# Kernel tuning notes

Measured on AMD Instinct MI355X. Metric: run time of the kernel, lower is better.

The kernel has to match this reference:

```python
import jax, jax.numpy as jnp
import numpy as np

HIDDEN = 2048
FFN = 1024
NUM_EXPERTS = 64
TOP_K = 8
TOTAL_EXPERTS = NUM_EXPERTS + TOP_K  # trash-can experts appended


def setup_inputs() -> dict:
    key = jax.random.key(0)
    ks = jax.random.split(key, 5)
    hidden_states = jax.random.normal(ks[0], (4, 2048, HIDDEN), dtype=jnp.float32)
    # gate: [total_experts, hidden]
    gate_w = jax.random.normal(ks[1], (TOTAL_EXPERTS, HIDDEN), dtype=jnp.float32) * 0.02
    # OlmoeMLP (SwiGLU): gate_proj, up_proj: [E, hidden, ffn]; down_proj: [E, ffn, hidden]
    w_gate = jax.random.normal(ks[2], (NUM_EXPERTS, HIDDEN, FFN), dtype=jnp.float32) * 0.02
    w_up = jax.random.normal(ks[3], (NUM_EXPERTS, HIDDEN, FFN), dtype=jnp.float32) * 0.02
    w_down = jax.random.normal(ks[4], (NUM_EXPERTS, FFN, HIDDEN), dtype=jnp.float32) * 0.02
    return {"hidden_states": hidden_states, "gate_w": gate_w,
            "w_gate": w_gate, "w_up": w_up, "w_down": w_down}


def _moe_forward(hidden_states, gate_w, w_gate, w_up, w_down):
    b, s, h = hidden_states.shape
    x = hidden_states.reshape(-1, h)  # [T, H]
    router_logits = x @ gate_w.T  # [T, total_experts]
    routing_weights = jax.nn.softmax(router_logits.astype(jnp.float32), axis=-1)
    topk_w, topk_idx = jax.lax.top_k(routing_weights, TOP_K)  # [T, K]
    # norm_topk_prob = False -> no renorm
    topk_w = topk_w.astype(hidden_states.dtype)

    # Dense-equivalent combine honoring sparsity via per-expert mask-weighted sum:
    # combine_w[t, e] = sum of topk weights where topk_idx==e, zero for trash experts.
    onehot = jax.nn.one_hot(topk_idx, TOTAL_EXPERTS, dtype=topk_w.dtype)  # [T,K,E_tot]
    combine_w = jnp.einsum('tk,tke->te', topk_w, onehot)[:, :NUM_EXPERTS]  # [T,E]

    # Grouped expert compute (vectorized over experts).
    # For correctness baseline we compute each expert on all tokens and weight;
    # zero weights kill non-routed tokens (same math as gather/scatter).
    def one_expert(wg, wu, wd, w_col):
        inter = jax.nn.silu(x @ wg) * (x @ wu)  # [T, FFN]
        return (inter @ wd) * w_col[:, None]    # [T, H]

    out = jnp.zeros_like(x)
    # scan over experts to cap peak memory at one [T,FFN] intermediate
    def body(acc, args):
        wg, wu, wd, w_col = args
        return acc + one_expert(wg, wu, wd, w_col), None
    out, _ = jax.lax.scan(body, out, (w_gate, w_up, w_down, combine_w.T))
    return out.reshape(b, s, h), router_logits


def reference(hidden_states, gate_w, w_gate, w_up, w_down):
    return _moe_forward(hidden_states, gate_w, w_gate, w_up, w_down)
```

## Files before the change

### kernel.cpp

```cpp
#include <hip/hip_runtime.h>
#include <hip/hip_bf16.h>
#include <stdint.h>

#define T_TOK 8192
#define HID   2048
#define FFN   1024
#define NEXP  64
#define ETOT  72
#define NPAD  80
#define TOPK  8
#define NASSIGN (T_TOK*TOPK)

typedef unsigned short u16;
typedef __bf16 bf16;
typedef bf16 bf16x8 __attribute__((ext_vector_type(8)));
typedef float f32x4 __attribute__((ext_vector_type(4)));

typedef const __attribute__((address_space(1))) void* gp_t;
typedef __attribute__((address_space(3))) void* lp_t;

__device__ __forceinline__ void gload16(const void* g, void* lds) {
  __builtin_amdgcn_global_load_lds((gp_t)g, (lp_t)lds, 16, 0, 0);
}
__device__ __forceinline__ f32x4 mfma16(bf16x8 a, bf16x8 b, f32x4 c) {
  return __builtin_amdgcn_mfma_f32_16x16x32_bf16(a, b, c, 0, 0, 0);
}

union U8 { bf16 h[8]; uint4 u; };
union U2 { bf16 h[2]; unsigned int u; };

__global__ void k_prep_x(const float* __restrict__ x, u16* __restrict__ xh,
                         u16* __restrict__ xl, int n8) {
  int i = blockIdx.x * blockDim.x + threadIdx.x;
  int stride = gridDim.x * blockDim.x;
  for (; i < n8; i += stride) {
    const float4* p = (const float4*)(x + (size_t)i * 8);
    float4 a = p[0], b = p[1];
    float f[8] = {a.x,a.y,a.z,a.w,b.x,b.y,b.z,b.w};
    U8 hh, ll;
#pragma unroll
    for (int j = 0; j < 8; j++) {
      bf16 h = (bf16)f[j];
      hh.h[j] = h;
      ll.h[j] = (bf16)(f[j] - (float)h);
    }
    ((uint4*)xh)[i] = hh.u;
    ((uint4*)xl)[i] = ll.u;
  }
}

__global__ void k_prep_gate(const float* __restrict__ gw, u16* __restrict__ gh,
                            u16* __restrict__ gl) {
  int e = blockIdx.x;
  for (int k8 = threadIdx.x; k8 < HID/8; k8 += blockDim.x) {
    U8 hh, ll;
    if (e < ETOT) {
      const float4* p = (const float4*)(gw + (size_t)e*HID + k8*8);
      float4 a = p[0], b = p[1];
      float f[8] = {a.x,a.y,a.z,a.w,b.x,b.y,b.z,b.w};
#pragma unroll
      for (int j = 0; j < 8; j++) {
        bf16 h = (bf16)f[j]; hh.h[j] = h; ll.h[j] = (bf16)(f[j]-(float)h);
      }
    } else {
      hh.u = make_uint4(0,0,0,0); ll.u = make_uint4(0,0,0,0);
    }
    ((uint4*)gh)[(size_t)e*(HID/8) + k8] = hh.u;
    ((uint4*)gl)[(size_t)e*(HID/8) + k8] = ll.u;
  }
}

__global__ void k_convT(const float* __restrict__ src, u16* __restrict__ dst,
                        int R, int C) {
  int e = blockIdx.z;
  src += (size_t)e * R * C;
  dst += (size_t)e * R * C;
  int c0 = blockIdx.x * 64, r0 = blockIdx.y * 128;
  __shared__ u16 t[64 * 132];
  int tid = threadIdx.x;
  int rr = tid >> 4, cc = (tid & 15) * 4;
#pragma unroll
  for (int it = 0; it < 8; it++) {
    int r = it * 16 + rr;
    float4 v = *(const float4*)(src + (size_t)(r0 + r) * C + c0 + cc);
    const float* f = &v.x;
#pragma unroll
    for (int i = 0; i < 4; i++) {
      U2 u; u.h[0] = (bf16)f[i]; u.h[1] = (bf16)0.f;
      t[(cc + i) * 132 + r] = (u16)(u.u & 0xffffu);
    }
  }
  __syncthreads();
  int n = tid >> 2, kb = (tid & 3) * 32;
  u16* drow = dst + (size_t)(c0 + n) * R + r0 + kb;
  const u16* srow = &t[n * 132 + kb];
#pragma unroll
  for (int j = 0; j < 2; j++) {
    uint2 a = *(const uint2*)&srow[j*16 + 0];
    uint2 b = *(const uint2*)&srow[j*16 + 4];
    uint2 c = *(const uint2*)&srow[j*16 + 8];
    uint2 d = *(const uint2*)&srow[j*16 + 12];
    *(uint4*)&drow[j*16]     = make_uint4(a.x, a.y, b.x, b.y);
    *(uint4*)&drow[j*16 + 8] = make_uint4(c.x, c.y, d.x, d.y);
  }
}

__global__ void k_router(const u16* __restrict__ xh, const u16* __restrict__ xl,
                         const u16* __restrict__ gh, const u16* __restrict__ gl,
                         float* __restrict__ logits_out, int* __restrict__ tk_idx,
                         float* __restrict__ tk_w, int* __restrict__ counts) {
  __shared__ u16 la_h[64*32], la_l[64*32], lb_h[NPAD*32], lb_l[NPAD*32];
  __shared__ float llog[64*NPAD];
  int tid = threadIdx.x, lane = tid & 63, wid = tid >> 6;
  int t0 = blockIdx.x * 64;
  int rsub = lane >> 2, csub = lane & 3;
  f32x4 acc[5] = {};
#pragma unroll 1
  for (int k0 = 0; k0 < HID; k0 += 32) {
    int arow = wid*16 + rsub;
    gload16(xh + (size_t)(t0+arow)*HID + k0 + csub*8, &la_h[wid*512]);
    gload16(xl + (size_t)(t0+arow)*HID + k0 + csub*8, &la_l[wid*512]);
    int brow = wid*16 + rsub;
    gload16(gh + (size_t)brow*HID + k0 + csub*8, &lb_h[wid*512]);
    gload16(gl + (size_t)brow*HID + k0 + csub*8, &lb_l[wid*512]);
    if (wid == 0) gload16(gh + (size_t)(64+rsub)*HID + k0 + csub*8, &lb_h[4*512]);
    if (wid == 1) gload16(gl + (size_t)(64+rsub)*HID + k0 + csub*8, &lb_l[4*512]);
    __syncthreads();
    int ar = wid*16 + (lane & 15);
    int ks = lane >> 4;
    bf16x8 ah = *(const bf16x8*)&la_h[ar*32 + ks*8];
    bf16x8 al = *(const bf16x8*)&la_l[ar*32 + ks*8];
#pragma unroll
    for (int nf = 0; nf < 5; nf++) {
      int br = nf*16 + (lane & 15);
      bf16x8 bh = *(const bf16x8*)&lb_h[br*32 + ks*8];
      bf16x8 bl = *(const bf16x8*)&lb_l[br*32 + ks*8];
      acc[nf] = mfma16(ah, bh, acc[nf]);
      acc[nf] = mfma16(ah, bl, acc[nf]);
      acc[nf] = mfma16(al, bh, acc[nf]);
    }
    __syncthreads();
  }
  {
    int q = lane >> 4, c = lane & 15;
#pragma unroll
    for (int nf = 0; nf < 5; nf++)
#pragma unroll
      for (int r = 0; r < 4; r++)
        llog[(wid*16 + q*4 + r)*NPAD + nf*16 + c] = acc[nf][r];
  }
  __syncthreads();
  if (tid < 64) {
    int t = t0 + tid;
    float* lg = &llog[tid*NPAD];
    float m = -1e30f;
    for (int e = 0; e < ETOT; e++) {
      float v = lg[e];
      logits_out[(size_t)t*ETOT + e] = v;
      m = fmaxf(m, v);
    }
    float s = 0.f;
    for (int e = 0; e < ETOT; e++) s += __expf(lg[e] - m);
    uint64_t m0 = 0; unsigned int m1 = 0;
    for (int k = 0; k < TOPK; k++) {
      float best = -1e30f; int bi = 0;
      for (int e = 0; e < ETOT; e++) {
        bool used = (e < 64) ? ((m0 >> e) & 1) : ((m1 >> (e-64)) & 1);
        float v = lg[e];
        if (!used && v > best) { best = v; bi = e; }
      }
      if (bi < 64) m0 |= (1ull << bi); else m1 |= (1u << (bi-64));
      tk_idx[t*TOPK + k] = bi;
      tk_w[t*TOPK + k] = __expf(best - m) / s;
      if (bi < NEXP) atomicAdd(&counts[bi], 1);
    }
  }
}

__global__ void k_scan(const int* __restrict__ counts, int* __restrict__ offsets,
                       int* __restrict__ cursors) {
  if (threadIdx.x == 0) {
    int s = 0;
    for (int e = 0; e < NEXP; e++) { offsets[e] = s; cursors[e] = s; s += counts[e]; }
  }
}

__global__ void k_build(const int* __restrict__ tk_idx, const float* __restrict__ tk_w,
                        int* __restrict__ cursors, int* __restrict__ rows,
                        float* __restrict__ rwgt) {
  int t = blockIdx.x * blockDim.x + threadIdx.x;
  if (t >= T_TOK) return;
#pragma unroll
  for (int k = 0; k < TOPK; k++) {
    int e = tk_idx[t*TOPK + k];
    if (e < NEXP) {
      int p = atomicAdd(&cursors[e], 1);
      rows[p] = t;
      rwgt[p] = tk_w[t*TOPK + k];
    }
  }
}

__launch_bounds__(256, 4)
__global__ void k_gate(const u16* __restrict__ xh, const u16* __restrict__ wT,
                       const int* __restrict__ counts, const int* __restrict__ offsets,
                       const int* __restrict__ rows, u16* __restrict__ gout) {
  int wgid = blockIdx.x;
  int xcd = wgid & 7, slot = wgid >> 3;
  int m = slot & 7, q = slot >> 3;
  int g = xcd * 64 + q;
  int e = g >> 3, nb = g & 7;
  int cnt = counts[e];
  if (cnt == 0) return;
  int off = offsets[e];
  int n0 = nb * 128;
  int tid = threadIdx.x, lane = tid & 63, wid = tid >> 6;
  int wm = (wid >> 1) * 64, wn = (wid & 1) * 64;
  __shared__ __align__(16) char smem[16384];
  u16* la = (u16*)smem;
  u16* lb = (u16*)(smem + 8192);
  u16* lout = (u16*)smem;
  int rsub = lane >> 2, csub = lane & 3;
  int swzc = csub ^ ((rsub >> 1) & 3);
  int nr1 = wid*16 + rsub, nr2 = nr1 + 64;
  const u16* gb1 = wT + ((size_t)e*FFN + n0 + nr1)*HID + swzc*8;
  const u16* gb2 = wT + ((size_t)e*FFN + n0 + nr2)*HID + swzc*8;

  for (int m0 = m * 128; m0 < cnt; m0 += 1024) {
    int tok1 = (m0 + nr1 < cnt) ? rows[off + m0 + nr1] : 0;
    int tok2 = (m0 + nr2 < cnt) ? rows[off + m0 + nr2] : 0;
    const u16* ga1 = xh + (size_t)tok1*HID + swzc*8;
    const u16* ga2 = xh + (size_t)tok2*HID + swzc*8;
    f32x4 acc[4][4] = {};
#pragma unroll 1
    for (int k0 = 0; k0 < HID; k0 += 32) {
      gload16(ga1 + k0, &la[wid*512]);
      gload16(ga2 + k0, &la[(wid+4)*512]);
      gload16(gb1 + k0, &lb[wid*512]);
      gload16(gb2 + k0, &lb[(wid+4)*512]);
      __syncthreads();
      bf16x8 afr[4], bfr[4];
#pragma unroll
      for (int i = 0; i < 4; i++) {
        int row = wm + i*16 + (lane & 15);
        int ch = (lane >> 4) ^ ((row >> 1) & 3);
        afr[i] = *(const bf16x8*)&la[row*32 + ch*8];
        int n = wn + i*16 + (lane & 15);
        int chb = (lane >> 4) ^ ((n >> 1) & 3);
        bfr[i] = *(const bf16x8*)&lb[n*32 + chb*8];
      }
#pragma unroll
      for (int nf = 0; nf < 4; nf++)
#pragma unroll
        for (int mf = 0; mf < 4; mf++)
          acc[mf][nf] = mfma16(afr[mf], bfr[nf], acc[mf][nf]);
      __syncthreads();
    }
#pragma unroll
    for (int pass = 0; pass < 2; pass++) {
      if ((wid >> 1) == pass) {
#pragma unroll
        for (int mf = 0; mf < 4; mf++)
#pragma unroll
          for (int nf = 0; nf < 4; nf++)
#pragma unroll
            for (int r = 0; r < 4; r++) {
              int row = mf*16 + (lane >> 4)*4 + r;
              int col = wn + nf*16 + (lane & 15);
              U2 t; t.h[0] = (bf16)acc[mf][nf][r]; t.h[1] = (bf16)0.f;
              lout[row*128 + col] = (u16)(t.u & 0xffffu);
            }
      }
      __syncthreads();
      for (int idx = tid; idx < 1024; idx += 256) {
        int row = idx >> 4, c16 = idx & 15;
        int grow = m0 + pass*64 + row;
        if (grow < cnt) {
          uint4 v = *(const uint4*)&lout[row*128 + c16*8];
          *(uint4*)&gout[(size_t)(off + grow)*FFN + n0 + c16*8] = v;
        }
      }
      __syncthreads();
    }
  }
}

__launch_bounds__(256, 4)
__global__ void k_up(const u16* __restrict__ xh, const u16* __restrict__ wT,
                     const int* __restrict__ counts, const int* __restrict__ offsets,
                     const int* __restrict__ rows, u16* __restrict__ inter) {
  int wgid = blockIdx.x;
  int xcd = wgid & 7, slot = wgid >> 3;
  int m = slot & 7, q = slot >> 3;
  int g = xcd * 64 + q;
  int e = g >> 3, nb = g & 7;
  int cnt = counts[e];
  if (cnt == 0) return;
  int off = offsets[e];
  int n0 = nb * 128;
  int tid = threadIdx.x, lane = tid & 63, wid = tid >> 6;
  int wm = (wid >> 1) * 64, wn = (wid & 1) * 64;
  __shared__ __align__(16) char smem[32768];
  u16* la = (u16*)smem;
  u16* lb = (u16*)(smem + 8192);
  u16* lg = (u16*)smem;
  u16* lout = (u16*)(smem + 16384);
  int rsub = lane >> 2, csub = lane & 3;
  int swzc = csub ^ ((rsub >> 1) & 3);
  int nr1 = wid*16 + rsub, nr2 = nr1 + 64;
  const u16* gb1 = wT + ((size_t)e*FFN + n0 + nr1)*HID + swzc*8;
  const u16* gb2 = wT + ((size_t)e*FFN + n0 + nr2)*HID + swzc*8;

  for (int m0 = m * 128; m0 < cnt; m0 += 1024) {
    int tok1 = (m0 + nr1 < cnt) ? rows[off + m0 + nr1] : 0;
    int tok2 = (m0 + nr2 < cnt) ? rows[off + m0 + nr2] : 0;
    const u16* ga1 = xh + (size_t)tok1*HID + swzc*8;
    const u16* ga2 = xh + (size_t)tok2*HID + swzc*8;
    f32x4 acc[4][4] = {};
#pragma unroll 1
    for (int k0 = 0; k0 < HID; k0 += 32) {
      gload16(ga1 + k0, &la[wid*512]);
      gload16(ga2 + k0, &la[(wid+4)*512]);
      gload16(gb1 + k0, &lb[wid*512]);
      gload16(gb2 + k0, &lb[(wid+4)*512]);
      __syncthreads();
      bf16x8 afr[4], bfr[4];
#pragma unroll
      for (int i = 0; i < 4; i++) {
        int row = wm + i*16 + (lane & 15);
        int ch = (lane >> 4) ^ ((row >> 1) & 3);
        afr[i] = *(const bf16x8*)&la[row*32 + ch*8];
        int n = wn + i*16 + (lane & 15);
        int chb = (lane >> 4) ^ ((n >> 1) & 3);
        bfr[i] = *(const bf16x8*)&lb[n*32 + chb*8];
      }
#pragma unroll
      for (int nf = 0; nf < 4; nf++)
#pragma unroll
        for (int mf = 0; mf < 4; mf++)
          acc[mf][nf] = mfma16(afr[mf], bfr[nf], acc[mf][nf]);
      __syncthreads();
    }
#pragma unroll
    for (int pass = 0; pass < 2; pass++) {
      for (int idx = tid; idx < 1024; idx += 256) {
        int row = idx >> 4, c16 = idx & 15;
        int grow = m0 + pass*64 + row;
        uint4 v = make_uint4(0,0,0,0);
        if (grow < cnt)
          v = *(const uint4*)&inter[(size_t)(off + grow)*FFN + n0 + c16*8];
        *(uint4*)&lg[row*128 + c16*8] = v;
      }
      __syncthreads();
      if ((wid >> 1) == pass) {
#pragma unroll
        for (int mf = 0; mf < 4; mf++)
#pragma unroll
          for (int nf = 0; nf < 4; nf++)
#pragma unroll
            for (int r = 0; r < 4; r++) {
              int row = mf*16 + (lane >> 4)*4 + r;
              int col = wn + nf*16 + (lane & 15);
              U2 gv; gv.u = (unsigned int)lg[row*128 + col];
              float gg = (float)gv.h[0];
              float v = gg / (1.f + __expf(-gg)) * acc[mf][nf][r];
              U2 t; t.h[0] = (bf16)v; t.h[1] = (bf16)0.f;
              lout[row*128 + col] = (u16)(t.u & 0xffffu);
            }
      }
      __syncthreads();
      for (int idx = tid; idx < 1024; idx += 256) {
        int row = idx >> 4, c16 = idx & 15;
        int grow = m0 + pass*64 + row;
        if (grow < cnt) {
          uint4 v = *(const uint4*)&lout[row*128 + c16*8];
          *(uint4*)&inter[(size_t)(off + grow)*FFN + n0 + c16*8] = v;
        }
      }
      __syncthreads();
    }
  }
}

__launch_bounds__(256, 4)
__global__ void k_expert_down(const u16* __restrict__ inter, const u16* __restrict__ wdT,
                              const int* __restrict__ counts, const int* __restrict__ offsets,
                              const int* __restrict__ rows, const float* __restrict__ rwgt,
                              float* __restrict__ out) {
  int wgid = blockIdx.x;
  int xcd = wgid & 7, slot = wgid >> 3;
  int m = slot & 3, q = slot >> 2;
  int g = xcd * 128 + q;
  int e = g >> 4, nb = g & 15;
  int cnt = counts[e];
  if (cnt == 0) return;
  int off = offsets[e];
  int n0 = nb * 128;
  int tid = threadIdx.x, lane = tid & 63, wid = tid >> 6;
  int wm = (wid >> 1) * 64, wn = (wid & 1) * 64;
  __shared__ u16 la[128*32], lb[128*32];
  __shared__ int rows_l[128];
  __shared__ float rw_l[128];
  int rsub = lane >> 2, csub = lane & 3;
  int swzc = csub ^ ((rsub >> 1) & 3);
  int nr1 = wid*16 + rsub, nr2 = nr1 + 64;
  const u16* gb1 = wdT + ((size_t)e*HID + n0 + nr1)*FFN + swzc*8;
  const u16* gb2 = wdT + ((size_t)e*HID + n0 + nr2)*FFN + swzc*8;

  for (int m0 = m * 128; m0 < cnt; m0 += 512) {
    __syncthreads();
    if (tid < 128) {
      int r = m0 + tid;
      rows_l[tid] = (r < cnt) ? rows[off + r] : 0;
      rw_l[tid]   = (r < cnt) ? rwgt[off + r] : 0.f;
    }
    const u16* ga1 = inter + (size_t)(off + m0 + nr1)*FFN + swzc*8;
    const u16* ga2 = inter + (size_t)(off + m0 + nr2)*FFN + swzc*8;
    f32x4 acc[4][4] = {};
#pragma unroll 1
    for (int k0 = 0; k0 < FFN; k0 += 32) {
      gload16(ga1 + k0, &la[wid*512]);
      gload16(ga2 + k0, &la[(wid+4)*512]);
      gload16(gb1 + k0, &lb[wid*512]);
      gload16(gb2 + k0, &lb[(wid+4)*512]);
      __syncthreads();
      bf16x8 afr[4], bfr[4];
#pragma unroll
      for (int i = 0; i < 4; i++) {
        int row = wm + i*16 + (lane & 15);
        int ch = (lane >> 4) ^ ((row >> 1) & 3);
        afr[i] = *(const bf16x8*)&la[row*32 + ch*8];
        int n = wn + i*16 + (lane & 15);
        int chb = (lane >> 4) ^ ((n >> 1) & 3);
        bfr[i] = *(const bf16x8*)&lb[n*32 + chb*8];
      }
#pragma unroll
      for (int nf = 0; nf < 4; nf++)
#pragma unroll
        for (int mf = 0; mf < 4; mf++)
          acc[mf][nf] = mfma16(afr[mf], bfr[nf], acc[mf][nf]);
      __syncthreads();
    }
#pragma unroll
    for (int mf = 0; mf < 4; mf++)
#pragma unroll
      for (int nf = 0; nf < 4; nf++)
#pragma unroll
        for (int r = 0; r < 4; r++) {
          int row = wm + mf*16 + (lane >> 4)*4 + r;
          if (m0 + row < cnt) {
            int tok = rows_l[row];
            float w = rw_l[row];
            int col = n0 + wn + nf*16 + (lane & 15);
            atomicAdd(&out[(size_t)tok*HID + col], w * acc[mf][nf][r]);
          }
        }
  }
}

extern "C" void kernel_launch(void* const* d_in, const int* in_sizes, int n_in,
                              void* d_out, int out_size, void* d_ws, size_t ws_size,
                              hipStream_t stream) {
  const float* x      = (const float*)d_in[0];
  const float* gate_w = (const float*)d_in[1];
  const float* wg     = (const float*)d_in[2];
  const float* wu     = (const float*)d_in[3];
  const float* wd     = (const float*)d_in[4];
  float* out = (float*)d_out;
  float* logits_out = out + (size_t)T_TOK * HID;

  char* w = (char*)d_ws;
  u16* xh = (u16*)w;            w += (size_t)T_TOK*HID*2;
  u16* xl = (u16*)w;            w += (size_t)T_TOK*HID*2;
  u16* gh = (u16*)w;            w += (size_t)NPAD*HID*2;
  u16* gl = (u16*)w;            w += (size_t)NPAD*HID*2;
  int* tk_idx = (int*)w;        w += (size_t)T_TOK*TOPK*4;
  float* tk_w = (float*)w;      w += (size_t)T_TOK*TOPK*4;
  int* counts = (int*)w;        w += 256;
  int* offsets = (int*)w;       w += 256;
  int* cursors = (int*)w;       w += 256;
  int* rows = (int*)w;          w += (size_t)NASSIGN*4;
  float* rwgt = (float*)w;      w += (size_t)NASSIGN*4;
  u16* inter = (u16*)w;         w += ((size_t)NASSIGN + 256)*FFN*2;
  u16* wgT = (u16*)w;           w += (size_t)NEXP*FFN*HID*2;
  u16* wuT = (u16*)w;           w += (size_t)NEXP*FFN*HID*2;
  u16* wdT = (u16*)w;

  hipMemsetAsync(d_out, 0, (size_t)T_TOK*HID*4, stream);
  hipMemsetAsync(counts, 0, 256, stream);

  k_prep_x<<<2048, 256, 0, stream>>>(x, xh, xl, T_TOK*HID/8);
  k_prep_gate<<<NPAD, 256, 0, stream>>>(gate_w, gh, gl);
  k_router<<<T_TOK/64, 256, 0, stream>>>(xh, xl, gh, gl, logits_out, tk_idx, tk_w, counts);
  k_scan<<<1, 64, 0, stream>>>(counts, offsets, cursors);
  k_build<<<T_TOK/256, 256, 0, stream>>>(tk_idx, tk_w, cursors, rows, rwgt);

  k_convT<<<dim3(FFN/64, HID/128, NEXP), 256, 0, stream>>>(wg, wgT, HID, FFN);
  k_convT<<<dim3(FFN/64, HID/128, NEXP), 256, 0, stream>>>(wu, wuT, HID, FFN);
  k_convT<<<dim3(HID/64, FFN/128, NEXP), 256, 0, stream>>>(wd, wdT, FFN, HID);

  k_gate<<<4096, 256, 0, stream>>>(xh, wgT, counts, offsets, rows, inter);
  k_up<<<4096, 256, 0, stream>>>(xh, wuT, counts, offsets, rows, inter);
  k_expert_down<<<4096, 256, 0, stream>>>(inter, wdT, counts, offsets, rows, rwgt, out);
}
```

Measured before the change: 1.959 ms.

## Fuse fp32 weight conversion into expert GEMMs with register-prefetched B tiles

Removes the separate transpose/convert kernels that turned the fp32 expert weights into transposed bf16 copies. Each GEMM now reads fp32 weights straight from global memory into registers, converts them to bf16 and writes them swizzled into LDS. The next K-slice is prefetched into registers while the current one is computed, with the main loop unrolled by two. This saves writing and re-reading about 800MB of converted weights, but each weight tile is now fetched as fp32 by every M-tile block. Register pressure rises, so launch bounds drop to 3 waves per SIMD.

```diff
diff --git a/kernel.cpp b/kernel.cpp
--- a/kernel.cpp
+++ b/kernel.cpp
@@ -67,41 +67,6 @@
     }
     ((uint4*)gh)[(size_t)e*(HID/8) + k8] = hh.u;
     ((uint4*)gl)[(size_t)e*(HID/8) + k8] = ll.u;
-  }
-}
-
-__global__ void k_convT(const float* __restrict__ src, u16* __restrict__ dst,
-                        int R, int C) {
-  int e = blockIdx.z;
-  src += (size_t)e * R * C;
-  dst += (size_t)e * R * C;
-  int c0 = blockIdx.x * 64, r0 = blockIdx.y * 128;
-  __shared__ u16 t[64 * 132];
-  int tid = threadIdx.x;
-  int rr = tid >> 4, cc = (tid & 15) * 4;
-#pragma unroll
-  for (int it = 0; it < 8; it++) {
-    int r = it * 16 + rr;
-    float4 v = *(const float4*)(src + (size_t)(r0 + r) * C + c0 + cc);
-    const float* f = &v.x;
-#pragma unroll
-    for (int i = 0; i < 4; i++) {
-      U2 u; u.h[0] = (bf16)f[i]; u.h[1] = (bf16)0.f;
-      t[(cc + i) * 132 + r] = (u16)(u.u & 0xffffu);
-    }
-  }
-  __syncthreads();
-  int n = tid >> 2, kb = (tid & 3) * 32;
-  u16* drow = dst + (size_t)(c0 + n) * R + r0 + kb;
-  const u16* srow = &t[n * 132 + kb];
-#pragma unroll
-  for (int j = 0; j < 2; j++) {
-    uint2 a = *(const uint2*)&srow[j*16 + 0];
-    uint2 b = *(const uint2*)&srow[j*16 + 4];
-    uint2 c = *(const uint2*)&srow[j*16 + 8];
-    uint2 d = *(const uint2*)&srow[j*16 + 12];
-    *(uint4*)&drow[j*16]     = make_uint4(a.x, a.y, b.x, b.y);
-    *(uint4*)&drow[j*16 + 8] = make_uint4(c.x, c.y, d.x, d.y);
   }
 }
 
@@ -201,10 +166,27 @@
   }
 }
 
-__launch_bounds__(256, 4)
-__global__ void k_gate(const u16* __restrict__ xh, const u16* __restrict__ wT,
+#define BLOAD(dst, K) do { \
+    _Pragma("unroll") \
+    for (int i = 0; i < 8; i++) { \
+      dst[i]   = pB[(size_t)((K) + cb*8 + i)     * BSTRIDE]; \
+      dst[8+i] = pB[(size_t)((K) + cb*8 + 8 + i) * BSTRIDE]; \
+    } \
+  } while (0)
+
+#define BWRITE(src) do { \
+    U8 p1, p2; \
+    _Pragma("unroll") \
+    for (int i = 0; i < 8; i++) { p1.h[i] = (bf16)src[i]; p2.h[i] = (bf16)src[8+i]; } \
+    *(uint4*)wp1 = p1.u; \
+    *(uint4*)wp2 = p2.u; \
+  } while (0)
+
+__launch_bounds__(256, 3)
+__global__ void k_gate(const u16* __restrict__ xh, const float* __restrict__ wg,
                        const int* __restrict__ counts, const int* __restrict__ offsets,
                        const int* __restrict__ rows, u16* __restrict__ gout) {
+#define BSTRIDE FFN
   int wgid = blockIdx.x;
   int xcd = wgid & 7, slot = wgid >> 3;
   int m = slot & 7, q = slot >> 3;
@@ -223,8 +205,28 @@
   int rsub = lane >> 2, csub = lane & 3;
   int swzc = csub ^ ((rsub >> 1) & 3);
   int nr1 = wid*16 + rsub, nr2 = nr1 + 64;
-  const u16* gb1 = wT + ((size_t)e*FFN + n0 + nr1)*HID + swzc*8;
-  const u16* gb2 = wT + ((size_t)e*FFN + n0 + nr2)*HID + swzc*8;
+  int bn = tid & 127, cb = (tid >> 7) * 2;
+  const float* pB = wg + (size_t)e*HID*FFN + n0 + bn;
+  u16* wp1 = &lb[bn*32 + ((cb    ) ^ ((bn>>1)&3))*8];
+  u16* wp2 = &lb[bn*32 + ((cb + 1) ^ ((bn>>1)&3))*8];
+
+#define G_COMPUTE() do { \
+    bf16x8 afr[4], bfr[4]; \
+    _Pragma("unroll") \
+    for (int i = 0; i < 4; i++) { \
+      int row = wm + i*16 + (lane & 15); \
+      int ch = (lane >> 4) ^ ((row >> 1) & 3); \
+      afr[i] = *(const bf16x8*)&la[row*32 + ch*8]; \
+      int n = wn + i*16 + (lane & 15); \
+      int chb = (lane >> 4) ^ ((n >> 1) & 3); \
+      bfr[i] = *(const bf16x8*)&lb[n*32 + chb*8]; \
+    } \
+    _Pragma("unroll") \
+    for (int nf = 0; nf < 4; nf++) \
+      _Pragma("unroll") \
+      for (int mf = 0; mf < 4; mf++) \
+        acc[mf][nf] = mfma16(afr[mf], bfr[nf], acc[mf][nf]); \
+  } while (0)
 
   for (int m0 = m * 128; m0 < cnt; m0 += 1024) {
     int tok1 = (m0 + nr1 < cnt) ? rows[off + m0 + nr1] : 0;
@@ -232,28 +234,23 @@
     const u16* ga1 = xh + (size_t)tok1*HID + swzc*8;
     const u16* ga2 = xh + (size_t)tok2*HID + swzc*8;
     f32x4 acc[4][4] = {};
+    float vb[16], vc[16];
+    BLOAD(vb, 0);
 #pragma unroll 1
-    for (int k0 = 0; k0 < HID; k0 += 32) {
+    for (int k0 = 0; k0 < HID; k0 += 64) {
+      BWRITE(vb);
       gload16(ga1 + k0, &la[wid*512]);
       gload16(ga2 + k0, &la[(wid+4)*512]);
-      gload16(gb1 + k0, &lb[wid*512]);
-      gload16(gb2 + k0, &lb[(wid+4)*512]);
-      __syncthreads();
-      bf16x8 afr[4], bfr[4];
-#pragma unroll
-      for (int i = 0; i < 4; i++) {
-        int row = wm + i*16 + (lane & 15);
-        int ch = (lane >> 4) ^ ((row >> 1) & 3);
-        afr[i] = *(const bf16x8*)&la[row*32 + ch*8];
-        int n = wn + i*16 + (lane & 15);
-        int chb = (lane >> 4) ^ ((n >> 1) & 3);
-        bfr[i] = *(const bf16x8*)&lb[n*32 + chb*8];
-      }
-#pragma unroll
-      for (int nf = 0; nf < 4; nf++)
-#pragma unroll
-        for (int mf = 0; mf < 4; mf++)
-          acc[mf][nf] = mfma16(afr[mf], bfr[nf], acc[mf][nf]);
+      __syncthreads();
+      BLOAD(vc, k0 + 32);
+      G_COMPUTE();
+      __syncthreads();
+      BWRITE(vc);
+      gload16(ga1 + k0 + 32, &la[wid*512]);
+      gload16(ga2 + k0 + 32, &la[(wid+4)*512]);
+      __syncthreads();
+      if (k0 + 64 < HID) BLOAD(vb, k0 + 64);
+      G_COMPUTE();
       __syncthreads();
     }
 #pragma unroll
@@ -283,12 +280,15 @@
       __syncthreads();
     }
   }
-}
-
-__launch_bounds__(256, 4)
-__global__ void k_up(const u16* __restrict__ xh, const u16* __restrict__ wT,
+#undef G_COMPUTE
+#undef BSTRIDE
+}
+
+__launch_bounds__(256, 3)
+__global__ void k_up(const u16* __restrict__ xh, const float* __restrict__ wu,
                      const int* __restrict__ counts, const int* __restrict__ offsets,
                      const int* __restrict__ rows, u16* __restrict__ inter) {
+#define BSTRIDE FFN
   int wgid = blockIdx.x;
   int xcd = wgid & 7, slot = wgid >> 3;
   int m = slot & 7, q = slot >> 3;
@@ -308,8 +308,28 @@
   int rsub = lane >> 2, csub = lane & 3;
   int swzc = csub ^ ((rsub >> 1) & 3);
   int nr1 = wid*16 + rsub, nr2 = nr1 + 64;
-  const u16* gb1 = wT + ((size_t)e*FFN + n0 + nr1)*HID + swzc*8;
-  const u16* gb2 = wT + ((size_t)e*FFN + n0 + nr2)*HID + swzc*8;
+  int bn = tid & 127, cb = (tid >> 7) * 2;
+  const float* pB = wu + (size_t)e*HID*FFN + n0 + bn;
+  u16* wp1 = &lb[bn*32 + ((cb    ) ^ ((bn>>1)&3))*8];
+  u16* wp2 = &lb[bn*32 + ((cb + 1) ^ ((bn>>1)&3))*8];
+
+#define U_COMPUTE() do { \
+    bf16x8 afr[4], bfr[4]; \
+    _Pragma("unroll") \
+    for (int i = 0; i < 4; i++) { \
+      int row = wm + i*16 + (lane & 15); \
+      int ch = (lane >> 4) ^ ((row >> 1) & 3); \
+      afr[i] = *(const bf16x8*)&la[row*32 + ch*8]; \
+      int n = wn + i*16 + (lane & 15); \
+      int chb = (lane >> 4) ^ ((n >> 1) & 3); \
+      bfr[i] = *(const bf16x8*)&lb[n*32 + chb*8]; \
+    } \
+    _Pragma("unroll") \
+    for (int nf = 0; nf < 4; nf++) \
+      _Pragma("unroll") \
+      for (int mf = 0; mf < 4; mf++) \
+        acc[mf][nf] = mfma16(afr[mf], bfr[nf], acc[mf][nf]); \
+  } while (0)
 
   for (int m0 = m * 128; m0 < cnt; m0 += 1024) {
     int tok1 = (m0 + nr1 < cnt) ? rows[off + m0 + nr1] : 0;
@@ -317,28 +337,23 @@
     const u16* ga1 = xh + (size_t)tok1*HID + swzc*8;
     const u16* ga2 = xh + (size_t)tok2*HID + swzc*8;
     f32x4 acc[4][4] = {};
+    float vb[16], vc[16];
+    BLOAD(vb, 0);
 #pragma unroll 1
-    for (int k0 = 0; k0 < HID; k0 += 32) {
+    for (int k0 = 0; k0 < HID; k0 += 64) {
+      BWRITE(vb);
       gload16(ga1 + k0, &la[wid*512]);
       gload16(ga2 + k0, &la[(wid+4)*512]);
-      gload16(gb1 + k0, &lb[wid*512]);
-      gload16(gb2 + k0, &lb[(wid+4)*512]);
-      __syncthreads();
-      bf16x8 afr[4], bfr[4];
-#pragma unroll
-      for (int i = 0; i < 4; i++) {
-        int row = wm + i*16 + (lane & 15);
-        int ch = (lane >> 4) ^ ((row >> 1) & 3);
-        afr[i] = *(const bf16x8*)&la[row*32 + ch*8];
-        int n = wn + i*16 + (lane & 15);
-        int chb = (lane >> 4) ^ ((n >> 1) & 3);
-        bfr[i] = *(const bf16x8*)&lb[n*32 + chb*8];
-      }
-#pragma unroll
-      for (int nf = 0; nf < 4; nf++)
-#pragma unroll
-        for (int mf = 0; mf < 4; mf++)
-          acc[mf][nf] = mfma16(afr[mf], bfr[nf], acc[mf][nf]);
+      __syncthreads();
+      BLOAD(vc, k0 + 32);
+      U_COMPUTE();
+      __syncthreads();
+      BWRITE(vc);
+      gload16(ga1 + k0 + 32, &la[wid*512]);
+      gload16(ga2 + k0 + 32, &la[(wid+4)*512]);
+      __syncthreads();
+      if (k0 + 64 < HID) BLOAD(vb, k0 + 64);
+      U_COMPUTE();
       __syncthreads();
     }
 #pragma unroll
@@ -380,13 +395,16 @@
       __syncthreads();
     }
   }
-}
-
-__launch_bounds__(256, 4)
-__global__ void k_expert_down(const u16* __restrict__ inter, const u16* __restrict__ wdT,
+#undef U_COMPUTE
+#undef BSTRIDE
+}
+
+__launch_bounds__(256, 3)
+__global__ void k_expert_down(const u16* __restrict__ inter, const float* __restrict__ wd,
                               const int* __restrict__ counts, const int* __restrict__ offsets,
                               const int* __restrict__ rows, const float* __restrict__ rwgt,
                               float* __restrict__ out) {
+#define BSTRIDE HID
   int wgid = blockIdx.x;
   int xcd = wgid & 7, slot = wgid >> 3;
   int m = slot & 3, q = slot >> 2;
@@ -398,14 +416,36 @@
   int n0 = nb * 128;
   int tid = threadIdx.x, lane = tid & 63, wid = tid >> 6;
   int wm = (wid >> 1) * 64, wn = (wid & 1) * 64;
-  __shared__ u16 la[128*32], lb[128*32];
+  __shared__ __align__(16) char smem[16384];
+  u16* la = (u16*)smem;
+  u16* lb = (u16*)(smem + 8192);
   __shared__ int rows_l[128];
   __shared__ float rw_l[128];
   int rsub = lane >> 2, csub = lane & 3;
   int swzc = csub ^ ((rsub >> 1) & 3);
   int nr1 = wid*16 + rsub, nr2 = nr1 + 64;
-  const u16* gb1 = wdT + ((size_t)e*HID + n0 + nr1)*FFN + swzc*8;
-  const u16* gb2 = wdT + ((size_t)e*HID + n0 + nr2)*FFN + swzc*8;
+  int bn = tid & 127, cb = (tid >> 7) * 2;
+  const float* pB = wd + (size_t)e*FFN*HID + n0 + bn;
+  u16* wp1 = &lb[bn*32 + ((cb    ) ^ ((bn>>1)&3))*8];
+  u16* wp2 = &lb[bn*32 + ((cb + 1) ^ ((bn>>1)&3))*8];
+
+#define D_COMPUTE() do { \
+    bf16x8 afr[4], bfr[4]; \
+    _Pragma("unroll") \
+    for (int i = 0; i < 4; i++) { \
+      int row = wm + i*16 + (lane & 15); \
+      int ch = (lane >> 4) ^ ((row >> 1) & 3); \
+      afr[i] = *(const bf16x8*)&la[row*32 + ch*8]; \
+      int n = wn + i*16 + (lane & 15); \
+      int chb = (lane >> 4) ^ ((n >> 1) & 3); \
+      bfr[i] = *(const bf16x8*)&lb[n*32 + chb*8]; \
+    } \
+    _Pragma("unroll") \
+    for (int nf = 0; nf < 4; nf++) \
+      _Pragma("unroll") \
+      for (int mf = 0; mf < 4; mf++) \
+        acc[mf][nf] = mfma16(afr[mf], bfr[nf], acc[mf][nf]); \
+  } while (0)
 
   for (int m0 = m * 128; m0 < cnt; m0 += 512) {
     __syncthreads();
@@ -417,28 +457,23 @@
     const u16* ga1 = inter + (size_t)(off + m0 + nr1)*FFN + swzc*8;
     const u16* ga2 = inter + (size_t)(off + m0 + nr2)*FFN + swzc*8;
     f32x4 acc[4][4] = {};
+    float vb[16], vc[16];
+    BLOAD(vb, 0);
 #pragma unroll 1
-    for (int k0 = 0; k0 < FFN; k0 += 32) {
+    for (int k0 = 0; k0 < FFN; k0 += 64) {
+      BWRITE(vb);
       gload16(ga1 + k0, &la[wid*512]);
       gload16(ga2 + k0, &la[(wid+4)*512]);
-      gload16(gb1 + k0, &lb[wid*512]);
-      gload16(gb2 + k0, &lb[(wid+4)*512]);
-      __syncthreads();
-      bf16x8 afr[4], bfr[4];
-#pragma unroll
-      for (int i = 0; i < 4; i++) {
-        int row = wm + i*16 + (lane & 15);
-        int ch = (lane >> 4) ^ ((row >> 1) & 3);
-        afr[i] = *(const bf16x8*)&la[row*32 + ch*8];
-        int n = wn + i*16 + (lane & 15);
-        int chb = (lane >> 4) ^ ((n >> 1) & 3);
-        bfr[i] = *(const bf16x8*)&lb[n*32 + chb*8];
-      }
-#pragma unroll
-      for (int nf = 0; nf < 4; nf++)
-#pragma unroll
-        for (int mf = 0; mf < 4; mf++)
-          acc[mf][nf] = mfma16(afr[mf], bfr[nf], acc[mf][nf]);
+      __syncthreads();
+      BLOAD(vc, k0 + 32);
+      D_COMPUTE();
+      __syncthreads();
+      BWRITE(vc);
+      gload16(ga1 + k0 + 32, &la[wid*512]);
+      gload16(ga2 + k0 + 32, &la[(wid+4)*512]);
+      __syncthreads();
+      if (k0 + 64 < FFN) BLOAD(vb, k0 + 64);
+      D_COMPUTE();
       __syncthreads();
     }
 #pragma unroll
@@ -456,6 +491,8 @@
           }
         }
   }
+#undef D_COMPUTE
+#undef BSTRIDE
 }
 
 extern "C" void kernel_launch(void* const* d_in, const int* in_sizes, int n_in,
@@ -481,10 +518,7 @@
   int* cursors = (int*)w;       w += 256;
   int* rows = (int*)w;          w += (size_t)NASSIGN*4;
   float* rwgt = (float*)w;      w += (size_t)NASSIGN*4;
-  u16* inter = (u16*)w;         w += ((size_t)NASSIGN + 256)*FFN*2;
-  u16* wgT = (u16*)w;           w += (size_t)NEXP*FFN*HID*2;
-  u16* wuT = (u16*)w;           w += (size_t)NEXP*FFN*HID*2;
-  u16* wdT = (u16*)w;
+  u16* inter = (u16*)w;
 
   hipMemsetAsync(d_out, 0, (size_t)T_TOK*HID*4, stream);
   hipMemsetAsync(counts, 0, 256, stream);
@@ -495,11 +529,7 @@
   k_scan<<<1, 64, 0, stream>>>(counts, offsets, cursors);
   k_build<<<T_TOK/256, 256, 0, stream>>>(tk_idx, tk_w, cursors, rows, rwgt);
 
-  k_convT<<<dim3(FFN/64, HID/128, NEXP), 256, 0, stream>>>(wg, wgT, HID, FFN);
-  k_convT<<<dim3(FFN/64, HID/128, NEXP), 256, 0, stream>>>(wu, wuT, HID, FFN);
-  k_convT<<<dim3(HID/64, FFN/128, NEXP), 256, 0, stream>>>(wd, wdT, FFN, HID);
-
-  k_gate<<<4096, 256, 0, stream>>>(xh, wgT, counts, offsets, rows, inter);
-  k_up<<<4096, 256, 0, stream>>>(xh, wuT, counts, offsets, rows, inter);
-  k_expert_down<<<4096, 256, 0, stream>>>(inter, wdT, counts, offsets, rows, rwgt, out);
-}
+  k_gate<<<4096, 256, 0, stream>>>(xh, wg, counts, offsets, rows, inter);
+  k_up<<<4096, 256, 0, stream>>>(xh, wu, counts, offsets, rows, inter);
+  k_expert_down<<<4096, 256, 0, stream>>>(inter, wd, counts, offsets, rows, rwgt, out);
+}
```

Result: no change. 1.994 ms (+1.8%).

## Replace atomic scatter in down-projection with bf16 scratch plus per-token combine

Applied to the files above, without the earlier changes.

The down-projection kernel now writes weighted per-assignment outputs as bf16 rows into a scratch buffer through LDS-staged coalesced stores, instead of doing fp32 atomicAdds into the output. A new combine kernel sums the top-k slots per token using a slot map recorded in k_build, and the output memset is dropped. This removes about 134M scattered float atomics but adds a 64K x 2048 bf16 scratch round trip, and rounding to bf16 before the sum loses some precision.

```diff
diff --git a/kernel.cpp b/kernel.cpp
--- a/kernel.cpp
+++ b/kernel.cpp
@@ -187,7 +187,7 @@
 
 __global__ void k_build(const int* __restrict__ tk_idx, const float* __restrict__ tk_w,
                         int* __restrict__ cursors, int* __restrict__ rows,
-                        float* __restrict__ rwgt) {
+                        float* __restrict__ rwgt, int* __restrict__ slots) {
   int t = blockIdx.x * blockDim.x + threadIdx.x;
   if (t >= T_TOK) return;
 #pragma unroll
@@ -197,6 +197,9 @@
       int p = atomicAdd(&cursors[e], 1);
       rows[p] = t;
       rwgt[p] = tk_w[t*TOPK + k];
+      slots[t*TOPK + k] = p;
+    } else {
+      slots[t*TOPK + k] = -1;
     }
   }
 }
@@ -385,8 +388,7 @@
 __launch_bounds__(256, 4)
 __global__ void k_expert_down(const u16* __restrict__ inter, const u16* __restrict__ wdT,
                               const int* __restrict__ counts, const int* __restrict__ offsets,
-                              const int* __restrict__ rows, const float* __restrict__ rwgt,
-                              float* __restrict__ out) {
+                              const float* __restrict__ rwgt, u16* __restrict__ dscratch) {
   int wgid = blockIdx.x;
   int xcd = wgid & 7, slot = wgid >> 3;
   int m = slot & 3, q = slot >> 2;
@@ -398,8 +400,10 @@
   int n0 = nb * 128;
   int tid = threadIdx.x, lane = tid & 63, wid = tid >> 6;
   int wm = (wid >> 1) * 64, wn = (wid & 1) * 64;
-  __shared__ u16 la[128*32], lb[128*32];
-  __shared__ int rows_l[128];
+  __shared__ __align__(16) char smem[16384];
+  u16* la = (u16*)smem;
+  u16* lb = (u16*)(smem + 8192);
+  u16* lout = (u16*)smem;
   __shared__ float rw_l[128];
   int rsub = lane >> 2, csub = lane & 3;
   int swzc = csub ^ ((rsub >> 1) & 3);
@@ -411,8 +415,7 @@
     __syncthreads();
     if (tid < 128) {
       int r = m0 + tid;
-      rows_l[tid] = (r < cnt) ? rows[off + r] : 0;
-      rw_l[tid]   = (r < cnt) ? rwgt[off + r] : 0.f;
+      rw_l[tid] = (r < cnt) ? rwgt[off + r] : 0.f;
     }
     const u16* ga1 = inter + (size_t)(off + m0 + nr1)*FFN + swzc*8;
     const u16* ga2 = inter + (size_t)(off + m0 + nr2)*FFN + swzc*8;
@@ -442,20 +445,57 @@
       __syncthreads();
     }
 #pragma unroll
-    for (int mf = 0; mf < 4; mf++)
-#pragma unroll
-      for (int nf = 0; nf < 4; nf++)
-#pragma unroll
-        for (int r = 0; r < 4; r++) {
-          int row = wm + mf*16 + (lane >> 4)*4 + r;
-          if (m0 + row < cnt) {
-            int tok = rows_l[row];
-            float w = rw_l[row];
-            int col = n0 + wn + nf*16 + (lane & 15);
-            atomicAdd(&out[(size_t)tok*HID + col], w * acc[mf][nf][r]);
-          }
+    for (int pass = 0; pass < 2; pass++) {
+      if ((wid >> 1) == pass) {
+#pragma unroll
+        for (int mf = 0; mf < 4; mf++)
+#pragma unroll
+          for (int nf = 0; nf < 4; nf++)
+#pragma unroll
+            for (int r = 0; r < 4; r++) {
+              int row = mf*16 + (lane >> 4)*4 + r;
+              int col = wn + nf*16 + (lane & 15);
+              float w = rw_l[pass*64 + row];
+              U2 t; t.h[0] = (bf16)(w * acc[mf][nf][r]); t.h[1] = (bf16)0.f;
+              lout[row*128 + col] = (u16)(t.u & 0xffffu);
+            }
+      }
+      __syncthreads();
+      for (int idx = tid; idx < 1024; idx += 256) {
+        int row = idx >> 4, c16 = idx & 15;
+        int grow = m0 + pass*64 + row;
+        if (grow < cnt) {
+          uint4 v = *(const uint4*)&lout[row*128 + c16*8];
+          *(uint4*)&dscratch[(size_t)(off + grow)*HID + n0 + c16*8] = v;
         }
-  }
+      }
+      __syncthreads();
+    }
+  }
+}
+
+__global__ void k_combine(const u16* __restrict__ dscratch, const int* __restrict__ slots,
+                          float* __restrict__ out) {
+  int t = blockIdx.x;
+  int tid = threadIdx.x;
+  __shared__ int sl[TOPK];
+  if (tid < TOPK) sl[tid] = slots[t*TOPK + tid];
+  __syncthreads();
+  int c = tid * 8;
+  float acc[8] = {0.f,0.f,0.f,0.f,0.f,0.f,0.f,0.f};
+#pragma unroll
+  for (int k = 0; k < TOPK; k++) {
+    int p = sl[k];
+    if (p >= 0) {
+      bf16x8 v = *(const bf16x8*)&dscratch[(size_t)p*HID + c];
+#pragma unroll
+      for (int i = 0; i < 8; i++) acc[i] += (float)v[i];
+    }
+  }
+  float4 o0 = make_float4(acc[0], acc[1], acc[2], acc[3]);
+  float4 o1 = make_float4(acc[4], acc[5], acc[6], acc[7]);
+  *(float4*)&out[(size_t)t*HID + c]     = o0;
+  *(float4*)&out[(size_t)t*HID + c + 4] = o1;
 }
 
 extern "C" void kernel_launch(void* const* d_in, const int* in_sizes, int n_in,
@@ -481,19 +521,20 @@
   int* cursors = (int*)w;       w += 256;
   int* rows = (int*)w;          w += (size_t)NASSIGN*4;
   float* rwgt = (float*)w;      w += (size_t)NASSIGN*4;
+  int* slots = (int*)w;         w += (size_t)NASSIGN*4;
   u16* inter = (u16*)w;         w += ((size_t)NASSIGN + 256)*FFN*2;
+  u16* dscratch = (u16*)w;      w += (size_t)NASSIGN*HID*2;
   u16* wgT = (u16*)w;           w += (size_t)NEXP*FFN*HID*2;
   u16* wuT = (u16*)w;           w += (size_t)NEXP*FFN*HID*2;
   u16* wdT = (u16*)w;
 
-  hipMemsetAsync(d_out, 0, (size_t)T_TOK*HID*4, stream);
   hipMemsetAsync(counts, 0, 256, stream);
 
   k_prep_x<<<2048, 256, 0, stream>>>(x, xh, xl, T_TOK*HID/8);
   k_prep_gate<<<NPAD, 256, 0, stream>>>(gate_w, gh, gl);
   k_router<<<T_TOK/64, 256, 0, stream>>>(xh, xl, gh, gl, logits_out, tk_idx, tk_w, counts);
   k_scan<<<1, 64, 0, stream>>>(counts, offsets, cursors);
-  k_build<<<T_TOK/256, 256, 0, stream>>>(tk_idx, tk_w, cursors, rows, rwgt);
+  k_build<<<T_TOK/256, 256, 0, stream>>>(tk_idx, tk_w, cursors, rows, rwgt, slots);
 
   k_convT<<<dim3(FFN/64, HID/128, NEXP), 256, 0, stream>>>(wg, wgT, HID, FFN);
   k_convT<<<dim3(FFN/64, HID/128, NEXP), 256, 0, stream>>>(wu, wuT, HID, FFN);
@@ -501,5 +542,6 @@
 
   k_gate<<<4096, 256, 0, stream>>>(xh, wgT, counts, offsets, rows, inter);
   k_up<<<4096, 256, 0, stream>>>(xh, wuT, counts, offsets, rows, inter);
-  k_expert_down<<<4096, 256, 0, stream>>>(inter, wdT, counts, offsets, rows, rwgt, out);
-}
+  k_expert_down<<<4096, 256, 0, stream>>>(inter, wdT, counts, offsets, rwgt, dscratch);
+  k_combine<<<T_TOK, 256, 0, stream>>>(dscratch, slots, out);
+}
```

Measured after the change: 1.814 ms. -7.4%, faster.
